# Kernel optimization log

Hardware: AMD Instinct MI355X
Metric: run time of the kernel (lower is better)

Reference implementation:

```python
import jax, jax.numpy as jnp
import numpy as np

NP, NQ, E, D = 100000, 50000, 600000, 128


def _seg_mean(x, idx, n):
    # mean aggregation per destination node (PyG scatter-mean, zero for isolated nodes)
    s = jax.ops.segment_sum(x, idx, num_segments=n)
    c = jax.ops.segment_sum(jnp.ones((idx.shape[0], 1), x.dtype), idx, num_segments=n)
    return s / jnp.maximum(c, 1.0)


def setup_inputs() -> dict:
    key = jax.random.key(0)
    ks = jax.random.split(key, 20)
    sc = 1.0 / np.sqrt(D)
    inp = {
        'x_person': jax.random.normal(ks[0], (NP, D), jnp.float32),
        'x_product': jax.random.normal(ks[1], (NQ, D), jnp.float32),
        'src_pv': jax.random.randint(ks[2], (E,), 0, NP, jnp.int32),
        'dst_pv': jax.random.randint(ks[3], (E,), 0, NQ, jnp.int32),
        'src_vp': jax.random.randint(ks[4], (E,), 0, NQ, jnp.int32),
        'dst_vp': jax.random.randint(ks[5], (E,), 0, NP, jnp.int32),
    }
    i = 6
    for layer in (0, 1):
        for et in ('pv', 'vp'):
            inp[f'Wl_{et}{layer}'] = jax.random.normal(ks[i], (D, D), jnp.float32) * sc; i += 1
            inp[f'Wr_{et}{layer}'] = jax.random.normal(ks[i], (D, D), jnp.float32) * sc; i += 1
            inp[f'b_{et}{layer}'] = jnp.zeros((D,), jnp.float32)
    return inp


def _layer(h_p, h_q, src_pv, dst_pv, src_vp, dst_vp, Wl_pv, Wr_pv, b_pv, Wl_vp, Wr_vp, b_vp):
    # SAGEConv per edge type: lin_l(mean_j x_src) + lin_r(x_dst) + bias; HeteroConv aggr='sum'
    agg_q = _seg_mean(h_p[src_pv], dst_pv, NQ)   # person -> product
    agg_p = _seg_mean(h_q[src_vp], dst_vp, NP)   # product -> person
    new_q = agg_q @ Wl_pv + h_q @ Wr_pv + b_pv
    new_p = agg_p @ Wl_vp + h_p @ Wr_vp + b_vp
    return new_p, new_q


def reference(x_person, x_product,
              Wl_pv0, Wr_pv0, b_pv0, Wl_vp0, Wr_vp0, b_vp0,
              Wl_pv1, Wr_pv1, b_pv1, Wl_vp1, Wr_vp1, b_vp1,
              src_pv, dst_pv, src_vp, dst_vp):
    h_p, h_q = _layer(x_person, x_product, src_pv, dst_pv, src_vp, dst_vp,
                      Wl_pv0, Wr_pv0, b_pv0, Wl_vp0, Wr_vp0, b_vp0)
    h_p, h_q = jax.nn.relu(h_p), jax.nn.relu(h_q)  # dropout identity (eval mode)
    h_p, h_q = _layer(h_p, h_q, src_pv, dst_pv, src_vp, dst_vp,
                      Wl_pv1, Wr_pv1, b_pv1, Wl_vp1, Wr_vp1, b_vp1)
    return h_p, h_q
```

## Files before the change

### kernel.cpp

```cpp
#include <hip/hip_runtime.h>

#define D 128
#define PAD 40
#define NBT 256
#define DNMAX 512
#define GT 32
#define GCAP 4096

typedef __attribute__((ext_vector_type(8))) short short8;
typedef __attribute__((ext_vector_type(4))) float f32x4;

__device__ __forceinline__ unsigned short f2bf(float x) {
    union { float f; unsigned u; } v; v.f = x;
    unsigned r = v.u + 0x7fff + ((v.u >> 16) & 1);
    return (unsigned short)(r >> 16);
}

__global__ __launch_bounds__(256) void prep_hist(
    const float* W0, const float* W1, const float* W2, const float* W3,
    const float* W4, const float* W5, const float* W6, const float* W7,
    unsigned short* __restrict__ wt,
    const int* __restrict__ dst_pv, const int* __restrict__ dst_vp, int E,
    int shq, int shp, int* __restrict__ bq, int* __restrict__ bp,
    const float* __restrict__ xp, unsigned short* __restrict__ xbp, int np4,
    const float* __restrict__ xq, unsigned short* __restrict__ xbq, int nq4) {
    int blk = blockIdx.x;
    int tid = threadIdx.x;
    if (blk < 64) {
        int m = blk >> 3;
        int c0 = (blk & 7) * 16;
        const float* W;
        switch (m) {
            case 0: W = W0; break; case 1: W = W1; break;
            case 2: W = W2; break; case 3: W = W3; break;
            case 4: W = W4; break; case 5: W = W5; break;
            case 6: W = W6; break; default: W = W7; break;
        }
        unsigned short* hi = wt + (size_t)m * 32768;
        unsigned short* lo = hi + 16384;

        __shared__ unsigned short his[16][136];
        __shared__ unsigned short los[16][136];
        int cc = tid & 15;
        int kk = tid >> 4;
        #pragma unroll
        for (int g = 0; g < 8; ++g) {
            int k = g * 16 + kk;
            float x = W[k * 128 + c0 + cc];
            unsigned short h = f2bf(x);
            union { float f; unsigned u; } hv; hv.u = ((unsigned)h) << 16;
            his[cc][k] = h;
            los[cc][k] = f2bf(x - hv.f);
        }
        __syncthreads();
        int cidx = tid >> 4;
        int k8   = (tid & 15) * 8;
        int c = c0 + cidx;
        uint4 vh, vl;
        #pragma unroll
        for (int j = 0; j < 4; ++j) {
            ((unsigned*)&vh)[j] = *(const unsigned*)&his[cidx][k8 + j * 2];
            ((unsigned*)&vl)[j] = *(const unsigned*)&los[cidx][k8 + j * 2];
        }
        *(uint4*)(hi + (size_t)c * 128 + k8) = vh;
        *(uint4*)(lo + (size_t)c * 128 + k8) = vl;
    } else if (blk < 320) {
        __shared__ int hq[NBT], hp[NBT];
        if (tid < NBT) { hq[tid] = 0; hp[tid] = 0; }
        __syncthreads();
        for (int e = (blk - 64) * 256 + tid; e < E; e += 256 * 256) {
            atomicAdd(&hq[dst_pv[e] >> shq], 1);
            atomicAdd(&hp[dst_vp[e] >> shp], 1);
        }
        __syncthreads();
        if (tid < NBT) {
            if (hq[tid]) atomicAdd(&bq[tid], hq[tid]);
            if (hp[tid]) atomicAdd(&bp[tid], hp[tid]);
        }
    } else {
        int tot = np4 + nq4;
        int stride = (gridDim.x - 320) * 256;
        for (int g = (blk - 320) * 256 + tid; g < tot; g += stride) {
            const float* src; unsigned short* dst; int i;
            if (g < np4) { src = xp; dst = xbp; i = g; }
            else         { src = xq; dst = xbq; i = g - np4; }
            float4 v = ((const float4*)src)[i];
            ushort4 o;
            o.x = f2bf(v.x); o.y = f2bf(v.y); o.z = f2bf(v.z); o.w = f2bf(v.w);
            ((ushort4*)dst)[i] = o;
        }
    }
}

__global__ __launch_bounds__(128) void bscan(int* __restrict__ bq, int nbq,
                                             int* __restrict__ bp, int nbp,
                                             int* __restrict__ curq, int* __restrict__ curp,
                                             int* __restrict__ rp_q, int nq,
                                             int* __restrict__ rp_p, int np, int E) {
    int wid = threadIdx.x >> 6, lane = threadIdx.x & 63;
    int* seg = wid ? bp : bq;
    int* cur = wid ? curp : curq;
    int nseg = wid ? nbp : nbq;
    int carry = 0;
    for (int base = 0; base < nseg; base += 64) {
        int i = base + lane;
        int v = (i < nseg) ? seg[i] : 0;
        int inc = v;
        #pragma unroll
        for (int off = 1; off < 64; off <<= 1) {
            int t = __shfl_up(inc, off, 64);
            if (lane >= off) inc += t;
        }
        if (i < nseg) { int ex = carry + inc - v; seg[i] = ex; cur[i] = ex; }
        carry += __shfl(inc, 63, 64);
    }
    if (lane == 0) { if (wid == 0) rp_q[nq] = E; else rp_p[np] = E; }
}

__global__ __launch_bounds__(256) void bscatter(const int* __restrict__ src_pv,
                                                const int* __restrict__ dst_pv,
                                                const int* __restrict__ src_vp,
                                                const int* __restrict__ dst_vp, int E,
                                                int* __restrict__ curq, int shq,
                                                int* __restrict__ curp, int shp,
                                                unsigned* __restrict__ pk_q,
                                                unsigned* __restrict__ pk_p) {
    __shared__ int cq[NBT], baq[NBT], wq[NBT];
    __shared__ int cp_[NBT], bap[NBT], wp_[NBT];
    int tid = threadIdx.x;
    int nblk = gridDim.x;
    int chunk = (E + nblk - 1) / nblk;
    int lo = blockIdx.x * chunk;
    int hi = min(lo + chunk, E);
    unsigned mkq = (1u << shq) - 1, mkp = (1u << shp) - 1;
    if (tid < NBT) { cq[tid] = 0; cp_[tid] = 0; }
    __syncthreads();
    for (int e = lo + tid; e < hi; e += 256) {
        atomicAdd(&cq[dst_pv[e] >> shq], 1);
        atomicAdd(&cp_[dst_vp[e] >> shp], 1);
    }
    __syncthreads();
    if (tid < NBT) {
        baq[tid] = cq[tid]  ? atomicAdd(&curq[tid], cq[tid])  : 0; wq[tid]  = 0;
        bap[tid] = cp_[tid] ? atomicAdd(&curp[tid], cp_[tid]) : 0; wp_[tid] = 0;
    }
    __syncthreads();
    for (int e = lo + tid; e < hi; e += 256) {
        int d = dst_pv[e]; int b = d >> shq;
        int off = atomicAdd(&wq[b], 1);
        pk_q[baq[b] + off] = ((unsigned)src_pv[e] << shq) | ((unsigned)d & mkq);
        d = dst_vp[e]; b = d >> shp;
        off = atomicAdd(&wp_[b], 1);
        pk_p[bap[b] + off] = ((unsigned)src_vp[e] << shp) | ((unsigned)d & mkp);
    }
}

__global__ __launch_bounds__(256) void bcsr(const unsigned* __restrict__ pk_q,
                                            const unsigned* __restrict__ pk_p,
                                            const int* __restrict__ bbq, int nbq,
                                            const int* __restrict__ bbp, int nbp,
                                            int* __restrict__ rp_q, int nq, int shq,
                                            int* __restrict__ rp_p, int np, int shp,
                                            int* __restrict__ col_q, int* __restrict__ col_p,
                                            int E) {
    int b = blockIdx.x;
    const unsigned* pk; const int* bb; int* rp; int* colg; int nb, n, sh;
    if (b < nbq) { pk = pk_q; bb = bbq; rp = rp_q; colg = col_q; nb = nbq; n = nq; sh = shq; }
    else { b -= nbq; pk = pk_p; bb = bbp; rp = rp_p; colg = col_p; nb = nbp; n = np; sh = shp; }
    int base = bb[b];
    int next = (b + 1 < nb) ? bb[b + 1] : E;
    int cnt = next - base;
    int dlo = b << sh;
    int dn  = min(1 << sh, n - dlo);
    unsigned mask = (1u << sh) - 1;

    __shared__ int deg[DNMAX];
    __shared__ int cur[DNMAX];
    __shared__ int wsum[4];
    int tid = threadIdx.x, lane = tid & 63, wid = tid >> 6;

    for (int i = tid; i < dn; i += 256) deg[i] = 0;
    __syncthreads();
    for (int i = tid; i < cnt; i += 256)
        atomicAdd(&deg[pk[base + i] & mask], 1);
    __syncthreads();

    int t2 = tid * 2;
    int d0 = (t2 < dn) ? deg[t2] : 0;
    int d1 = (t2 + 1 < dn) ? deg[t2 + 1] : 0;
    int s = d0 + d1;
    int inc = s;
    #pragma unroll
    for (int off = 1; off < 64; off <<= 1) {
        int t = __shfl_up(inc, off, 64);
        if (lane >= off) inc += t;
    }
    if (lane == 63) wsum[wid] = inc;
    __syncthreads();
    int wpre = 0;
    for (int w2 = 0; w2 < wid; ++w2) wpre += wsum[w2];
    int ex = wpre + inc - s;
    if (t2 < dn)     { cur[t2] = ex;           rp[dlo + t2] = base + ex; }
    if (t2 + 1 < dn) { cur[t2 + 1] = ex + d0;  rp[dlo + t2 + 1] = base + ex + d0; }
    __syncthreads();

    for (int i = tid; i < cnt; i += 256) {
        unsigned v = pk[base + i];
        int off = atomicAdd(&cur[v & mask], 1);
        colg[base + off] = (int)(v >> sh);
    }
}

__global__ __launch_bounds__(256) void agg_all(
    const int* __restrict__ rp_q, const int* __restrict__ col_q,
    const unsigned short* __restrict__ srcq, unsigned short* __restrict__ outq, int nq,
    const int* __restrict__ rp_p, const int* __restrict__ col_p,
    const unsigned short* __restrict__ srcp, unsigned short* __restrict__ outp, int np,
    int ntq) {
    __shared__ int rps[GT + 1];
    __shared__ int cols[GCAP];

    int blk = blockIdx.x;
    const int* rp; const int* col; const unsigned short* src; unsigned short* out; int n, d0;
    if (blk < ntq) { rp = rp_q; col = col_q; src = srcq; out = outq; n = nq; d0 = blk * GT; }
    else { rp = rp_p; col = col_p; src = srcp; out = outp; n = np; d0 = (blk - ntq) * GT; }

    int tid = threadIdx.x;
    int nrow = min(GT, n - d0);
    if (tid <= nrow) rps[tid] = rp[d0 + tid];
    __syncthreads();
    int beg0 = rps[0];
    int cnt = rps[nrow] - beg0;
    bool useLds = cnt <= GCAP;
    if (useLds)
        for (int i = tid; i < cnt; i += 256) cols[i] = col[beg0 + i];
    __syncthreads();

    int wid = tid >> 6, lane = tid & 63;
    int sub = lane >> 4;
    int ch  = lane & 15;

    for (int r = wid; r < nrow; r += 4) {
        int beg = rps[r], end = rps[r + 1];
        float a0 = 0.f, a1 = 0.f, a2 = 0.f, a3 = 0.f;
        float a4 = 0.f, a5 = 0.f, a6 = 0.f, a7 = 0.f;
        for (int i = beg; i < end; i += 16) {
            uint4 v[4]; bool act[4];
            #pragma unroll
            for (int h2 = 0; h2 < 4; ++h2) {
                int j = i + h2 * 4 + sub;
                act[h2] = j < end;
                if (act[h2]) {
                    int s = useLds ? cols[j - beg0] : col[j];
                    v[h2] = *(const uint4*)(src + (size_t)s * D + ch * 8);
                }
            }
            #pragma unroll
            for (int h2 = 0; h2 < 4; ++h2) {
                if (act[h2]) {
                    union { unsigned u; float f; } t;
                    t.u = v[h2].x << 16;         a0 += t.f;
                    t.u = v[h2].x & 0xffff0000u; a1 += t.f;
                    t.u = v[h2].y << 16;         a2 += t.f;
                    t.u = v[h2].y & 0xffff0000u; a3 += t.f;
                    t.u = v[h2].z << 16;         a4 += t.f;
                    t.u = v[h2].z & 0xffff0000u; a5 += t.f;
                    t.u = v[h2].w << 16;         a6 += t.f;
                    t.u = v[h2].w & 0xffff0000u; a7 += t.f;
                }
            }
        }
        #pragma unroll
        for (int off = 16; off <= 32; off <<= 1) {
            a0 += __shfl_xor(a0, off); a1 += __shfl_xor(a1, off);
            a2 += __shfl_xor(a2, off); a3 += __shfl_xor(a3, off);
            a4 += __shfl_xor(a4, off); a5 += __shfl_xor(a5, off);
            a6 += __shfl_xor(a6, off); a7 += __shfl_xor(a7, off);
        }
        int deg = end - beg;
        float inv = (deg > 0) ? 1.0f / (float)deg : 0.f;
        if (sub == 0) {
            uint4 o;
            o.x = (unsigned)f2bf(a0 * inv) | ((unsigned)f2bf(a1 * inv) << 16);
            o.y = (unsigned)f2bf(a2 * inv) | ((unsigned)f2bf(a3 * inv) << 16);
            o.z = (unsigned)f2bf(a4 * inv) | ((unsigned)f2bf(a5 * inv) << 16);
            o.w = (unsigned)f2bf(a6 * inv) | ((unsigned)f2bf(a7 * inv) << 16);
            *(uint4*)(out + (size_t)(d0 + r) * D + ch * 8) = o;
        }
    }
}

struct GemmSide {
    const unsigned short* A1;
    const unsigned short* A2;
    const unsigned short* Wt1;
    const unsigned short* Wt2;
    const float* bias;
    float* out;
    unsigned short* hb;
    int n;
};

template <bool RELU, bool WF32, bool WHB>
__device__ __forceinline__ void gemm_body(const GemmSide& S, int bidx) {
    __shared__ unsigned short As[128][PAD];
    __shared__ unsigned short Ws_hi[128][PAD];
    __shared__ unsigned short Ws_lo[128][PAD];

    const int tid  = threadIdx.x;
    const int lane = tid & 63;
    const int w    = tid >> 6;
    const int m0   = bidx * 128;
    const int n    = S.n;

    f32x4 acc[2][8];
    #pragma unroll
    for (int i = 0; i < 2; ++i)
        #pragma unroll
        for (int j = 0; j < 8; ++j) acc[i][j] = (f32x4)0.f;

    const int srow  = tid >> 1;
    const int skoff = (tid & 1) * 16;

    for (int ks = 0; ks < 8; ++ks) {
        const int half = ks >> 2;
        const int kb   = (ks & 3) * 32;
        const unsigned short* A  = half ? S.A2 : S.A1;
        const unsigned short* Wt = half ? S.Wt2 : S.Wt1;

        {
            int grow = m0 + srow;
            if (grow >= n) grow = n - 1;
            const uint4* pa = (const uint4*)(A + (size_t)grow * D + kb + skoff);
            ((uint4*)&As[srow][skoff])[0] = pa[0];
            ((uint4*)&As[srow][skoff])[1] = pa[1];
        }
        {
            const uint4* ph = (const uint4*)(Wt + (size_t)srow * D + kb + skoff);
            ((uint4*)&Ws_hi[srow][skoff])[0] = ph[0];
            ((uint4*)&Ws_hi[srow][skoff])[1] = ph[1];
            const uint4* pl = (const uint4*)(Wt + 16384 + (size_t)srow * D + kb + skoff);
            ((uint4*)&Ws_lo[srow][skoff])[0] = pl[0];
            ((uint4*)&Ws_lo[srow][skoff])[1] = pl[1];
        }
        __syncthreads();

        const int r0 = w * 32;
        const int k8 = (lane >> 4) * 8;
        const int li = lane & 15;

        short8 ah[2];
        #pragma unroll
        for (int m = 0; m < 2; ++m)
            ah[m] = *(const short8*)&As[r0 + m * 16 + li][k8];
        #pragma unroll
        for (int nb = 0; nb < 8; ++nb) {
            int cc = nb * 16 + li;
            short8 bh = *(const short8*)&Ws_hi[cc][k8];
            short8 bl = *(const short8*)&Ws_lo[cc][k8];
            #pragma unroll
            for (int m = 0; m < 2; ++m) {
                acc[m][nb] = __builtin_amdgcn_mfma_f32_16x16x32_bf16(ah[m], bh, acc[m][nb], 0, 0, 0);
                acc[m][nb] = __builtin_amdgcn_mfma_f32_16x16x32_bf16(ah[m], bl, acc[m][nb], 0, 0, 0);
            }
        }
        __syncthreads();
    }

    const int li = lane & 15;
    const int rq = (lane >> 4) * 4;
    float bv[8];
    #pragma unroll
    for (int nb = 0; nb < 8; ++nb) bv[nb] = S.bias[nb * 16 + li];

    #pragma unroll
    for (int m = 0; m < 2; ++m) {
        #pragma unroll
        for (int nb = 0; nb < 8; ++nb) {
            #pragma unroll
            for (int r = 0; r < 4; ++r) {
                int R = m0 + w * 32 + m * 16 + rq + r;
                if (R < n) {
                    int C = nb * 16 + li;
                    float v = acc[m][nb][r] + bv[nb];
                    if (RELU) v = fmaxf(v, 0.f);
                    if (WF32) S.out[(size_t)R * D + C] = v;
                    if (WHB)  S.hb[(size_t)R * D + C] = f2bf(v);
                }
            }
        }
    }
}

template <bool RELU, bool WF32, bool WHB>
__global__ __launch_bounds__(256) void gemm_both(GemmSide Sq, GemmSide Sp, int mq) {
    if ((int)blockIdx.x < mq) gemm_body<RELU, WF32, WHB>(Sq, blockIdx.x);
    else                      gemm_body<RELU, WF32, WHB>(Sp, blockIdx.x - mq);
}

extern "C" void kernel_launch(void* const* d_in, const int* in_sizes, int n_in,
                              void* d_out, int out_size, void* d_ws, size_t ws_size,
                              hipStream_t stream) {
    const float* x_p = (const float*)d_in[0];
    const float* x_q = (const float*)d_in[1];
    const int* src_pv = (const int*)d_in[2];
    const int* dst_pv = (const int*)d_in[3];
    const int* src_vp = (const int*)d_in[4];
    const int* dst_vp = (const int*)d_in[5];
    const float* Wl_pv0 = (const float*)d_in[6];
    const float* Wr_pv0 = (const float*)d_in[7];
    const float* b_pv0  = (const float*)d_in[8];
    const float* Wl_vp0 = (const float*)d_in[9];
    const float* Wr_vp0 = (const float*)d_in[10];
    const float* b_vp0  = (const float*)d_in[11];
    const float* Wl_pv1 = (const float*)d_in[12];
    const float* Wr_pv1 = (const float*)d_in[13];
    const float* b_pv1  = (const float*)d_in[14];
    const float* Wl_vp1 = (const float*)d_in[15];
    const float* Wr_vp1 = (const float*)d_in[16];
    const float* b_vp1  = (const float*)d_in[17];

    const int NP = in_sizes[0] / D;
    const int NQ = in_sizes[1] / D;
    const int E  = in_sizes[2];

    float* out_p = (float*)d_out;
    float* out_q = out_p + (size_t)NP * D;

    int shq = 6; while ((((NQ - 1) >> shq) + 1) > NBT) ++shq;
    int shp = 6; while ((((NP - 1) >> shp) + 1) > NBT) ++shp;
    int nbq = ((NQ - 1) >> shq) + 1;
    int nbp = ((NP - 1) >> shp) + 1;

    char* ws = (char*)d_ws;
    int* rp_q  = (int*)ws;
    int* rp_p  = rp_q + (NQ + 1);
    int* col_q = rp_p + (NP + 1);
    int* col_p = col_q + E;
    int* bq    = col_p + E;
    int* bp    = bq + NBT;
    int* curq  = bp + NBT;
    int* curp  = curq + NBT;
    size_t int_bytes = ((size_t)(NQ + 1) + (NP + 1) + 2 * (size_t)E + 4 * NBT) * sizeof(int);
    int_bytes = (int_bytes + 511) & ~(size_t)511;
    unsigned short* wt = (unsigned short*)(ws + int_bytes);
    size_t wt_bytes = ((size_t)8 * 32768 * sizeof(unsigned short) + 511) & ~(size_t)511;
    unsigned short* xb_p = (unsigned short*)(ws + int_bytes + wt_bytes);
    unsigned short* xb_q = xb_p + (size_t)NP * D;
    unsigned short* hb_p = xb_p;
    unsigned short* hb_q = xb_q;
    unsigned short* aggb_q = xb_q + (size_t)NQ * D;
    unsigned short* aggb_p = aggb_q + (size_t)NQ * D;
    unsigned* pk_q = (unsigned*)aggb_q;
    unsigned* pk_p = pk_q + E;

    hipMemsetAsync(bq, 0, 2 * NBT * sizeof(int), stream);
    prep_hist<<<320 + 2048, 256, 0, stream>>>(Wl_pv0, Wr_pv0, Wl_vp0, Wr_vp0,
                                              Wl_pv1, Wr_pv1, Wl_vp1, Wr_vp1, wt,
                                              dst_pv, dst_vp, E, shq, shp, bq, bp,
                                              x_p, xb_p, NP * D / 4, x_q, xb_q, NQ * D / 4);

    bscan<<<1, 128, 0, stream>>>(bq, nbq, bp, nbp, curq, curp, rp_q, NQ, rp_p, NP, E);
    bscatter<<<512, 256, 0, stream>>>(src_pv, dst_pv, src_vp, dst_vp, E,
                                      curq, shq, curp, shp, pk_q, pk_p);
    bcsr<<<nbq + nbp, 256, 0, stream>>>(pk_q, pk_p, bq, nbq, bp, nbp,
                                        rp_q, NQ, shq, rp_p, NP, shp, col_q, col_p, E);

    int ntq = (NQ + GT - 1) / GT, ntp = (NP + GT - 1) / GT;
    int mq = (NQ + 127) / 128, mp = (NP + 127) / 128;

    GemmSide Sq0 = { aggb_q, xb_q, wt + 0 * 32768, wt + 1 * 32768, b_pv0, out_q, hb_q, NQ };
    GemmSide Sp0 = { aggb_p, xb_p, wt + 2 * 32768, wt + 3 * 32768, b_vp0, out_p, hb_p, NP };
    GemmSide Sq1 = { aggb_q, hb_q, wt + 4 * 32768, wt + 5 * 32768, b_pv1, out_q, nullptr, NQ };
    GemmSide Sp1 = { aggb_p, hb_p, wt + 6 * 32768, wt + 7 * 32768, b_vp1, out_p, nullptr, NP };

    agg_all<<<ntq + ntp, 256, 0, stream>>>(rp_q, col_q, xb_p, aggb_q, NQ,
                                           rp_p, col_p, xb_q, aggb_p, NP, ntq);
    gemm_both<true, false, true><<<mq + mp, 256, 0, stream>>>(Sq0, Sp0, mq);

    agg_all<<<ntq + ntp, 256, 0, stream>>>(rp_q, col_q, hb_p, aggb_q, NQ,
                                           rp_p, col_p, hb_q, aggb_p, NP, ntq);
    gemm_both<false, true, false><<<mq + mp, 256, 0, stream>>>(Sq1, Sp1, mq);
}
```

Before: 251.6 us.

## Fuse fp32-to-bf16 input conversion into layer-0 aggregation and GEMM loads

Removes the standalone pass converting input node features to bf16; layer-0 aggregation now gathers fp32 rows directly and the layer-0 GEMM converts its fp32 root-feature operand to bf16 while loading tiles. Aggregation kernels become persistent grid-stride loops over tiles with a fixed 2048-block grid, and the LDS column cache shrinks to raise occupancy. This saves a full read/write pass over the inputs but doubles the bytes fetched by the layer-0 random gather.

```diff
diff --git a/kernel.cpp b/kernel.cpp
--- a/kernel.cpp
+++ b/kernel.cpp
@@ -5,7 +5,7 @@
 #define NBT 256
 #define DNMAX 512
 #define GT 32
-#define GCAP 4096
+#define GCAP 1536
 
 typedef __attribute__((ext_vector_type(8))) short short8;
 typedef __attribute__((ext_vector_type(4))) float f32x4;
@@ -21,9 +21,7 @@
     const float* W4, const float* W5, const float* W6, const float* W7,
     unsigned short* __restrict__ wt,
     const int* __restrict__ dst_pv, const int* __restrict__ dst_vp, int E,
-    int shq, int shp, int* __restrict__ bq, int* __restrict__ bp,
-    const float* __restrict__ xp, unsigned short* __restrict__ xbp, int np4,
-    const float* __restrict__ xq, unsigned short* __restrict__ xbq, int nq4) {
+    int shq, int shp, int* __restrict__ bq, int* __restrict__ bp) {
     int blk = blockIdx.x;
     int tid = threadIdx.x;
     if (blk < 64) {
@@ -64,7 +62,7 @@
         }
         *(uint4*)(hi + (size_t)c * 128 + k8) = vh;
         *(uint4*)(lo + (size_t)c * 128 + k8) = vl;
-    } else if (blk < 320) {
+    } else {
         __shared__ int hq[NBT], hp[NBT];
         if (tid < NBT) { hq[tid] = 0; hp[tid] = 0; }
         __syncthreads();
@@ -76,18 +74,6 @@
         if (tid < NBT) {
             if (hq[tid]) atomicAdd(&bq[tid], hq[tid]);
             if (hp[tid]) atomicAdd(&bp[tid], hp[tid]);
-        }
-    } else {
-        int tot = np4 + nq4;
-        int stride = (gridDim.x - 320) * 256;
-        for (int g = (blk - 320) * 256 + tid; g < tot; g += stride) {
-            const float* src; unsigned short* dst; int i;
-            if (g < np4) { src = xp; dst = xbp; i = g; }
-            else         { src = xq; dst = xbq; i = g - np4; }
-            float4 v = ((const float4*)src)[i];
-            ushort4 o;
-            o.x = f2bf(v.x); o.y = f2bf(v.y); o.z = f2bf(v.z); o.w = f2bf(v.w);
-            ((ushort4*)dst)[i] = o;
         }
     }
 }
@@ -211,88 +197,169 @@
     }
 }
 
-__global__ __launch_bounds__(256) void agg_all(
+__global__ __launch_bounds__(256) void agg_l0(
+    const int* __restrict__ rp_q, const int* __restrict__ col_q,
+    const float* __restrict__ srcq, unsigned short* __restrict__ outq, int nq,
+    const int* __restrict__ rp_p, const int* __restrict__ col_p,
+    const float* __restrict__ srcp, unsigned short* __restrict__ outp, int np,
+    int ntq, int ntot) {
+    __shared__ int rps[GT + 1];
+    __shared__ int cols[GCAP];
+
+    int tid = threadIdx.x;
+    int wid = tid >> 6, lane = tid & 63;
+    int sub = lane >> 4;
+    int ch  = lane & 15;
+
+    for (int tile = blockIdx.x; tile < ntot; tile += gridDim.x) {
+        const int* rp; const int* col; const float* src; unsigned short* out; int n, d0;
+        if (tile < ntq) { rp = rp_q; col = col_q; src = srcq; out = outq; n = nq; d0 = tile * GT; }
+        else { rp = rp_p; col = col_p; src = srcp; out = outp; n = np; d0 = (tile - ntq) * GT; }
+
+        int nrow = min(GT, n - d0);
+        if (tid <= nrow) rps[tid] = rp[d0 + tid];
+        __syncthreads();
+        int beg0 = rps[0];
+        int cnt = rps[nrow] - beg0;
+        bool useLds = cnt <= GCAP;
+        if (useLds)
+            for (int i = tid; i < cnt; i += 256) cols[i] = col[beg0 + i];
+        __syncthreads();
+
+        for (int r = wid; r < nrow; r += 4) {
+            int beg = rps[r], end = rps[r + 1];
+            float a0 = 0.f, a1 = 0.f, a2 = 0.f, a3 = 0.f;
+            float a4 = 0.f, a5 = 0.f, a6 = 0.f, a7 = 0.f;
+            for (int i = beg; i < end; i += 8) {
+                float4 v[2][2]; bool act[2];
+                #pragma unroll
+                for (int h2 = 0; h2 < 2; ++h2) {
+                    int j = i + h2 * 4 + sub;
+                    act[h2] = j < end;
+                    if (act[h2]) {
+                        int s = useLds ? cols[j - beg0] : col[j];
+                        const float* row = src + (size_t)s * D + ch * 8;
+                        v[h2][0] = ((const float4*)row)[0];
+                        v[h2][1] = ((const float4*)row)[1];
+                    }
+                }
+                #pragma unroll
+                for (int h2 = 0; h2 < 2; ++h2) {
+                    if (act[h2]) {
+                        a0 += v[h2][0].x; a1 += v[h2][0].y;
+                        a2 += v[h2][0].z; a3 += v[h2][0].w;
+                        a4 += v[h2][1].x; a5 += v[h2][1].y;
+                        a6 += v[h2][1].z; a7 += v[h2][1].w;
+                    }
+                }
+            }
+            #pragma unroll
+            for (int off = 16; off <= 32; off <<= 1) {
+                a0 += __shfl_xor(a0, off); a1 += __shfl_xor(a1, off);
+                a2 += __shfl_xor(a2, off); a3 += __shfl_xor(a3, off);
+                a4 += __shfl_xor(a4, off); a5 += __shfl_xor(a5, off);
+                a6 += __shfl_xor(a6, off); a7 += __shfl_xor(a7, off);
+            }
+            int deg = end - beg;
+            float inv = (deg > 0) ? 1.0f / (float)deg : 0.f;
+            if (sub == 0) {
+                uint4 o;
+                o.x = (unsigned)f2bf(a0 * inv) | ((unsigned)f2bf(a1 * inv) << 16);
+                o.y = (unsigned)f2bf(a2 * inv) | ((unsigned)f2bf(a3 * inv) << 16);
+                o.z = (unsigned)f2bf(a4 * inv) | ((unsigned)f2bf(a5 * inv) << 16);
+                o.w = (unsigned)f2bf(a6 * inv) | ((unsigned)f2bf(a7 * inv) << 16);
+                *(uint4*)(out + (size_t)(d0 + r) * D + ch * 8) = o;
+            }
+        }
+        __syncthreads();
+    }
+}
+
+__global__ __launch_bounds__(256) void agg_l1(
     const int* __restrict__ rp_q, const int* __restrict__ col_q,
     const unsigned short* __restrict__ srcq, unsigned short* __restrict__ outq, int nq,
     const int* __restrict__ rp_p, const int* __restrict__ col_p,
     const unsigned short* __restrict__ srcp, unsigned short* __restrict__ outp, int np,
-    int ntq) {
+    int ntq, int ntot) {
     __shared__ int rps[GT + 1];
     __shared__ int cols[GCAP];
 
-    int blk = blockIdx.x;
-    const int* rp; const int* col; const unsigned short* src; unsigned short* out; int n, d0;
-    if (blk < ntq) { rp = rp_q; col = col_q; src = srcq; out = outq; n = nq; d0 = blk * GT; }
-    else { rp = rp_p; col = col_p; src = srcp; out = outp; n = np; d0 = (blk - ntq) * GT; }
-
     int tid = threadIdx.x;
-    int nrow = min(GT, n - d0);
-    if (tid <= nrow) rps[tid] = rp[d0 + tid];
-    __syncthreads();
-    int beg0 = rps[0];
-    int cnt = rps[nrow] - beg0;
-    bool useLds = cnt <= GCAP;
-    if (useLds)
-        for (int i = tid; i < cnt; i += 256) cols[i] = col[beg0 + i];
-    __syncthreads();
-
     int wid = tid >> 6, lane = tid & 63;
     int sub = lane >> 4;
     int ch  = lane & 15;
 
-    for (int r = wid; r < nrow; r += 4) {
-        int beg = rps[r], end = rps[r + 1];
-        float a0 = 0.f, a1 = 0.f, a2 = 0.f, a3 = 0.f;
-        float a4 = 0.f, a5 = 0.f, a6 = 0.f, a7 = 0.f;
-        for (int i = beg; i < end; i += 16) {
-            uint4 v[4]; bool act[4];
+    for (int tile = blockIdx.x; tile < ntot; tile += gridDim.x) {
+        const int* rp; const int* col; const unsigned short* src; unsigned short* out; int n, d0;
+        if (tile < ntq) { rp = rp_q; col = col_q; src = srcq; out = outq; n = nq; d0 = tile * GT; }
+        else { rp = rp_p; col = col_p; src = srcp; out = outp; n = np; d0 = (tile - ntq) * GT; }
+
+        int nrow = min(GT, n - d0);
+        if (tid <= nrow) rps[tid] = rp[d0 + tid];
+        __syncthreads();
+        int beg0 = rps[0];
+        int cnt = rps[nrow] - beg0;
+        bool useLds = cnt <= GCAP;
+        if (useLds)
+            for (int i = tid; i < cnt; i += 256) cols[i] = col[beg0 + i];
+        __syncthreads();
+
+        for (int r = wid; r < nrow; r += 4) {
+            int beg = rps[r], end = rps[r + 1];
+            float a0 = 0.f, a1 = 0.f, a2 = 0.f, a3 = 0.f;
+            float a4 = 0.f, a5 = 0.f, a6 = 0.f, a7 = 0.f;
+            for (int i = beg; i < end; i += 16) {
+                uint4 v[4]; bool act[4];
+                #pragma unroll
+                for (int h2 = 0; h2 < 4; ++h2) {
+                    int j = i + h2 * 4 + sub;
+                    act[h2] = j < end;
+                    if (act[h2]) {
+                        int s = useLds ? cols[j - beg0] : col[j];
+                        v[h2] = *(const uint4*)(src + (size_t)s * D + ch * 8);
+                    }
+                }
+                #pragma unroll
+                for (int h2 = 0; h2 < 4; ++h2) {
+                    if (act[h2]) {
+                        union { unsigned u; float f; } t;
+                        t.u = v[h2].x << 16;         a0 += t.f;
+                        t.u = v[h2].x & 0xffff0000u; a1 += t.f;
+                        t.u = v[h2].y << 16;         a2 += t.f;
+                        t.u = v[h2].y & 0xffff0000u; a3 += t.f;
+                        t.u = v[h2].z << 16;         a4 += t.f;
+                        t.u = v[h2].z & 0xffff0000u; a5 += t.f;
+                        t.u = v[h2].w << 16;         a6 += t.f;
+                        t.u = v[h2].w & 0xffff0000u; a7 += t.f;
+                    }
+                }
+            }
             #pragma unroll
-            for (int h2 = 0; h2 < 4; ++h2) {
-                int j = i + h2 * 4 + sub;
-                act[h2] = j < end;
-                if (act[h2]) {
-                    int s = useLds ? cols[j - beg0] : col[j];
-                    v[h2] = *(const uint4*)(src + (size_t)s * D + ch * 8);
-                }
-            }
-            #pragma unroll
-            for (int h2 = 0; h2 < 4; ++h2) {
-                if (act[h2]) {
-                    union { unsigned u; float f; } t;
-                    t.u = v[h2].x << 16;         a0 += t.f;
-                    t.u = v[h2].x & 0xffff0000u; a1 += t.f;
-                    t.u = v[h2].y << 16;         a2 += t.f;
-                    t.u = v[h2].y & 0xffff0000u; a3 += t.f;
-                    t.u = v[h2].z << 16;         a4 += t.f;
-                    t.u = v[h2].z & 0xffff0000u; a5 += t.f;
-                    t.u = v[h2].w << 16;         a6 += t.f;
-                    t.u = v[h2].w & 0xffff0000u; a7 += t.f;
-                }
-            }
-        }
-        #pragma unroll
-        for (int off = 16; off <= 32; off <<= 1) {
-            a0 += __shfl_xor(a0, off); a1 += __shfl_xor(a1, off);
-            a2 += __shfl_xor(a2, off); a3 += __shfl_xor(a3, off);
-            a4 += __shfl_xor(a4, off); a5 += __shfl_xor(a5, off);
-            a6 += __shfl_xor(a6, off); a7 += __shfl_xor(a7, off);
-        }
-        int deg = end - beg;
-        float inv = (deg > 0) ? 1.0f / (float)deg : 0.f;
-        if (sub == 0) {
-            uint4 o;
-            o.x = (unsigned)f2bf(a0 * inv) | ((unsigned)f2bf(a1 * inv) << 16);
-            o.y = (unsigned)f2bf(a2 * inv) | ((unsigned)f2bf(a3 * inv) << 16);
-            o.z = (unsigned)f2bf(a4 * inv) | ((unsigned)f2bf(a5 * inv) << 16);
-            o.w = (unsigned)f2bf(a6 * inv) | ((unsigned)f2bf(a7 * inv) << 16);
-            *(uint4*)(out + (size_t)(d0 + r) * D + ch * 8) = o;
-        }
+            for (int off = 16; off <= 32; off <<= 1) {
+                a0 += __shfl_xor(a0, off); a1 += __shfl_xor(a1, off);
+                a2 += __shfl_xor(a2, off); a3 += __shfl_xor(a3, off);
+                a4 += __shfl_xor(a4, off); a5 += __shfl_xor(a5, off);
+                a6 += __shfl_xor(a6, off); a7 += __shfl_xor(a7, off);
+            }
+            int deg = end - beg;
+            float inv = (deg > 0) ? 1.0f / (float)deg : 0.f;
+            if (sub == 0) {
+                uint4 o;
+                o.x = (unsigned)f2bf(a0 * inv) | ((unsigned)f2bf(a1 * inv) << 16);
+                o.y = (unsigned)f2bf(a2 * inv) | ((unsigned)f2bf(a3 * inv) << 16);
+                o.z = (unsigned)f2bf(a4 * inv) | ((unsigned)f2bf(a5 * inv) << 16);
+                o.w = (unsigned)f2bf(a6 * inv) | ((unsigned)f2bf(a7 * inv) << 16);
+                *(uint4*)(out + (size_t)(d0 + r) * D + ch * 8) = o;
+            }
+        }
+        __syncthreads();
     }
 }
 
 struct GemmSide {
     const unsigned short* A1;
     const unsigned short* A2;
+    const float* A2f;
     const unsigned short* Wt1;
     const unsigned short* Wt2;
     const float* bias;
@@ -301,7 +368,7 @@
     int n;
 };
 
-template <bool RELU, bool WF32, bool WHB>
+template <bool RELU, bool WF32, bool WHB, bool A2F32>
 __device__ __forceinline__ void gemm_body(const GemmSide& S, int bidx) {
     __shared__ unsigned short As[128][PAD];
     __shared__ unsigned short Ws_hi[128][PAD];
@@ -325,15 +392,34 @@
     for (int ks = 0; ks < 8; ++ks) {
         const int half = ks >> 2;
         const int kb   = (ks & 3) * 32;
-        const unsigned short* A  = half ? S.A2 : S.A1;
         const unsigned short* Wt = half ? S.Wt2 : S.Wt1;
 
         {
             int grow = m0 + srow;
             if (grow >= n) grow = n - 1;
-            const uint4* pa = (const uint4*)(A + (size_t)grow * D + kb + skoff);
-            ((uint4*)&As[srow][skoff])[0] = pa[0];
-            ((uint4*)&As[srow][skoff])[1] = pa[1];
+            if (A2F32 && half) {
+                const float* ap = S.A2f + (size_t)grow * D + kb + skoff;
+                float4 u0 = ((const float4*)ap)[0];
+                float4 u1 = ((const float4*)ap)[1];
+                float4 u2 = ((const float4*)ap)[2];
+                float4 u3 = ((const float4*)ap)[3];
+                uint4 o0, o1;
+                o0.x = (unsigned)f2bf(u0.x) | ((unsigned)f2bf(u0.y) << 16);
+                o0.y = (unsigned)f2bf(u0.z) | ((unsigned)f2bf(u0.w) << 16);
+                o0.z = (unsigned)f2bf(u1.x) | ((unsigned)f2bf(u1.y) << 16);
+                o0.w = (unsigned)f2bf(u1.z) | ((unsigned)f2bf(u1.w) << 16);
+                o1.x = (unsigned)f2bf(u2.x) | ((unsigned)f2bf(u2.y) << 16);
+                o1.y = (unsigned)f2bf(u2.z) | ((unsigned)f2bf(u2.w) << 16);
+                o1.z = (unsigned)f2bf(u3.x) | ((unsigned)f2bf(u3.y) << 16);
+                o1.w = (unsigned)f2bf(u3.z) | ((unsigned)f2bf(u3.w) << 16);
+                ((uint4*)&As[srow][skoff])[0] = o0;
+                ((uint4*)&As[srow][skoff])[1] = o1;
+            } else {
+                const unsigned short* A = half ? S.A2 : S.A1;
+                const uint4* pa = (const uint4*)(A + (size_t)grow * D + kb + skoff);
+                ((uint4*)&As[srow][skoff])[0] = pa[0];
+                ((uint4*)&As[srow][skoff])[1] = pa[1];
+            }
         }
         {
             const uint4* ph = (const uint4*)(Wt + (size_t)srow * D + kb + skoff);
@@ -392,10 +478,10 @@
     }
 }
 
-template <bool RELU, bool WF32, bool WHB>
+template <bool RELU, bool WF32, bool WHB, bool A2F32>
 __global__ __launch_bounds__(256) void gemm_both(GemmSide Sq, GemmSide Sp, int mq) {
-    if ((int)blockIdx.x < mq) gemm_body<RELU, WF32, WHB>(Sq, blockIdx.x);
-    else                      gemm_body<RELU, WF32, WHB>(Sp, blockIdx.x - mq);
+    if ((int)blockIdx.x < mq) gemm_body<RELU, WF32, WHB, A2F32>(Sq, blockIdx.x);
+    else                      gemm_body<RELU, WF32, WHB, A2F32>(Sp, blockIdx.x - mq);
 }
 
 extern "C" void kernel_launch(void* const* d_in, const int* in_sizes, int n_in,
@@ -445,20 +531,17 @@
     int_bytes = (int_bytes + 511) & ~(size_t)511;
     unsigned short* wt = (unsigned short*)(ws + int_bytes);
     size_t wt_bytes = ((size_t)8 * 32768 * sizeof(unsigned short) + 511) & ~(size_t)511;
-    unsigned short* xb_p = (unsigned short*)(ws + int_bytes + wt_bytes);
-    unsigned short* xb_q = xb_p + (size_t)NP * D;
-    unsigned short* hb_p = xb_p;
-    unsigned short* hb_q = xb_q;
-    unsigned short* aggb_q = xb_q + (size_t)NQ * D;
+    unsigned short* hb_p = (unsigned short*)(ws + int_bytes + wt_bytes);
+    unsigned short* hb_q = hb_p + (size_t)NP * D;
+    unsigned short* aggb_q = hb_q + (size_t)NQ * D;
     unsigned short* aggb_p = aggb_q + (size_t)NQ * D;
     unsigned* pk_q = (unsigned*)aggb_q;
     unsigned* pk_p = pk_q + E;
 
     hipMemsetAsync(bq, 0, 2 * NBT * sizeof(int), stream);
-    prep_hist<<<320 + 2048, 256, 0, stream>>>(Wl_pv0, Wr_pv0, Wl_vp0, Wr_vp0,
-                                              Wl_pv1, Wr_pv1, Wl_vp1, Wr_vp1, wt,
-                                              dst_pv, dst_vp, E, shq, shp, bq, bp,
-                                              x_p, xb_p, NP * D / 4, x_q, xb_q, NQ * D / 4);
+    prep_hist<<<320, 256, 0, stream>>>(Wl_pv0, Wr_pv0, Wl_vp0, Wr_vp0,
+                                       Wl_pv1, Wr_pv1, Wl_vp1, Wr_vp1, wt,
+                                       dst_pv, dst_vp, E, shq, shp, bq, bp);
 
     bscan<<<1, 128, 0, stream>>>(bq, nbq, bp, nbp, curq, curp, rp_q, NQ, rp_p, NP, E);
     bscatter<<<512, 256, 0, stream>>>(src_pv, dst_pv, src_vp, dst_vp, E,
@@ -469,16 +552,16 @@
     int ntq = (NQ + GT - 1) / GT, ntp = (NP + GT - 1) / GT;
     int mq = (NQ + 127) / 128, mp = (NP + 127) / 128;
 
-    GemmSide Sq0 = { aggb_q, xb_q, wt + 0 * 32768, wt + 1 * 32768, b_pv0, out_q, hb_q, NQ };
-    GemmSide Sp0 = { aggb_p, xb_p, wt + 2 * 32768, wt + 3 * 32768, b_vp0, out_p, hb_p, NP };
-    GemmSide Sq1 = { aggb_q, hb_q, wt + 4 * 32768, wt + 5 * 32768, b_pv1, out_q, nullptr, NQ };
-    GemmSide Sp1 = { aggb_p, hb_p, wt + 6 * 32768, wt + 7 * 32768, b_vp1, out_p, nullptr, NP };
-
-    agg_all<<<ntq + ntp, 256, 0, stream>>>(rp_q, col_q, xb_p, aggb_q, NQ,
-                                           rp_p, col_p, xb_q, aggb_p, NP, ntq);
-    gemm_both<true, false, true><<<mq + mp, 256, 0, stream>>>(Sq0, Sp0, mq);
-
-    agg_all<<<ntq + ntp, 256, 0, stream>>>(rp_q, col_q, hb_p, aggb_q, NQ,
-                                           rp_p, col_p, hb_q, aggb_p, NP, ntq);
-    gemm_both<false, true, false><<<mq + mp, 256, 0, stream>>>(Sq1, Sp1, mq);
-}
+    GemmSide Sq0 = { aggb_q, nullptr, x_q, wt + 0 * 32768, wt + 1 * 32768, b_pv0, out_q, hb_q, NQ };
+    GemmSide Sp0 = { aggb_p, nullptr, x_p, wt + 2 * 32768, wt + 3 * 32768, b_vp0, out_p, hb_p, NP };
+    GemmSide Sq1 = { aggb_q, hb_q, nullptr, wt + 4 * 32768, wt + 5 * 32768, b_pv1, out_q, nullptr, NQ };
+    GemmSide Sp1 = { aggb_p, hb_p, nullptr, wt + 6 * 32768, wt + 7 * 32768, b_vp1, out_p, nullptr, NP };
+
+    agg_l0<<<2048, 256, 0, stream>>>(rp_q, col_q, x_p, aggb_q, NQ,
+                                     rp_p, col_p, x_q, aggb_p, NP, ntq, ntq + ntp);
+    gemm_both<true, false, true, true><<<mq + mp, 256, 0, stream>>>(Sq0, Sp0, mq);
+
+    agg_l1<<<2048, 256, 0, stream>>>(rp_q, col_q, hb_p, aggb_q, NQ,
+                                     rp_p, col_p, hb_q, aggb_p, NP, ntq, ntq + ntp);
+    gemm_both<false, true, false, false><<<mq + mp, 256, 0, stream>>>(Sq1, Sp1, mq);
+}
```

Result: slower. 304.4 us (+21.0%).
